# Kernel optimization log

Measured on AMD Instinct MI355X. Metric: run time of the kernel, lower is better.

The kernel has to match this reference:

```python
import jax, jax.numpy as jnp
import numpy as np

N_NODES = 524288
N_EDGES = 2097152
N_GRAPHS = 16384
COMP_DIM = 3539
PROT_DIM = 384
GNN_HID = 64
G_EMB = 128
HID = 256


def setup_inputs() -> dict:
    key = jax.random.key(0)
    ks = jax.random.split(key, 16)
    def lin(k, fan_in, fan_out):
        b = 1.0 / np.sqrt(fan_in)
        kw, kb = jax.random.split(k)
        return (jax.random.uniform(kw, (fan_in, fan_out), jnp.float32, -b, b),
                jax.random.uniform(kb, (fan_out,), jnp.float32, -b, b))
    W1, b1 = lin(ks[0], 1, GNN_HID)
    W2, b2 = lin(ks[1], GNN_HID, GNN_HID)
    Wg, bg = lin(ks[2], GNN_HID, G_EMB)
    Wf1, bf1 = lin(ks[3], G_EMB + COMP_DIM + PROT_DIM, HID)
    Wf2, bf2 = lin(ks[4], HID, 1)
    node_x = jax.random.normal(ks[5], (N_NODES, 1), jnp.float32)
    compound_feat = jax.random.normal(ks[6], (N_GRAPHS, COMP_DIM), jnp.float32)
    protein_feat = jax.random.normal(ks[7], (N_GRAPHS, PROT_DIM), jnp.float32)
    edge_index = jax.random.randint(ks[8], (2, N_EDGES), 0, N_NODES, jnp.int64 if jax.config.jax_enable_x64 else jnp.int32)
    batch = jnp.sort(jax.random.randint(ks[9], (N_NODES,), 0, N_GRAPHS, jnp.int32))
    return {"node_x": node_x, "compound_feat": compound_feat, "protein_feat": protein_feat,
            "edge_index": edge_index, "batch": batch,
            "W1": W1, "b1": b1, "W2": W2, "b2": b2, "Wg": Wg, "bg": bg,
            "Wf1": Wf1, "bf1": bf1, "Wf2": Wf2, "bf2": bf2}


def _gcn_norm(edge_index, num_nodes):
    # add self-loops, then symmetric normalization (PyG GCNConv default)
    loop = jnp.arange(num_nodes, dtype=edge_index.dtype)
    row = jnp.concatenate([edge_index[0], loop])
    col = jnp.concatenate([edge_index[1], loop])
    deg = jax.ops.segment_sum(jnp.ones_like(col, jnp.float32), col, num_segments=num_nodes)
    dinv = jnp.where(deg > 0, jax.lax.rsqrt(deg), 0.0)
    norm = dinv[row] * dinv[col]
    return row, col, norm


def _gcn_conv(x, W, b, row, col, norm, num_nodes):
    h = x @ W  # [N, out]
    out = jax.ops.segment_sum(norm[:, None] * h[row], col, num_segments=num_nodes)
    return out + b


def reference(node_x, compound_feat, protein_feat, edge_index, batch,
              W1, b1, W2, b2, Wg, bg, Wf1, bf1, Wf2, bf2):
    N = node_x.shape[0]
    B = compound_feat.shape[0]
    row, col, norm = _gcn_norm(edge_index, N)
    x = jax.nn.relu(_gcn_conv(node_x, W1, b1, row, col, norm, N))
    x = jax.nn.relu(_gcn_conv(x, W2, b2, row, col, norm, N))
    # global mean pool per graph
    sums = jax.ops.segment_sum(x, batch, num_segments=B)
    cnts = jax.ops.segment_sum(jnp.ones((N,), jnp.float32), batch, num_segments=B)
    pooled = sums / jnp.maximum(cnts, 1.0)[:, None]
    g = pooled @ Wg + bg  # [B, G_EMB]
    combined = jnp.concatenate([g, compound_feat, protein_feat], axis=1)
    h = jax.nn.relu(combined @ Wf1 + bf1)
    return jax.nn.sigmoid(h @ Wf2 + bf2)
```

## Files before the change

kernel.cpp:

```cpp
#include <hip/hip_runtime.h>

#define NN 524288
#define NE 2097152
#define NG 16384
#define CDIM 3539
#define PDIM 384
#define GH 64
#define GE 128
#define HIDD 256
#define KD (GE + CDIM + PDIM)
#define KP 4096

typedef short bf16x8 __attribute__((ext_vector_type(8)));
typedef unsigned short u16x8 __attribute__((ext_vector_type(8)));
typedef float f32x4 __attribute__((ext_vector_type(4)));

__device__ inline unsigned short f2bf(float f) {
    unsigned int u = __float_as_uint(f);
    u += 0x7FFF + ((u >> 16) & 1);
    return (unsigned short)(u >> 16);
}

__global__ void k_init(int* __restrict__ idg, float* __restrict__ sums) {
    int i = blockIdx.x * blockDim.x + threadIdx.x;
    if (i < NN) idg[i] = 0;
    if (i < NG * GH) sums[i] = 0.0f;
}

__global__ void k_deg(const int* __restrict__ ei, int* __restrict__ idg,
                      int* __restrict__ eseq) {
    int e = blockIdx.x * blockDim.x + threadIdx.x;
    eseq[e] = atomicAdd(&idg[ei[NE + e]], 1);
}

__global__ void k_prep(const float* __restrict__ node_x, const int* __restrict__ idg,
                       float2* __restrict__ f2a, int* __restrict__ ecnt) {
    int n = blockIdx.x * blockDim.x + threadIdx.x;
    int c = idg[n];
    float di = rsqrtf((float)(c + 1));
    f2a[n] = make_float2(di * node_x[n], di);
    ecnt[n] = c;
}

__global__ void k_cnt(const int* __restrict__ batch, float* __restrict__ cnt) {
    int g = blockIdx.x * 256 + threadIdx.x;
    int lo = 0, hi = NN;
    while (lo < hi) { int mid = (lo + hi) >> 1; if (batch[mid] < g) lo = mid + 1; else hi = mid; }
    int lo2 = lo, hi2 = NN;
    while (lo2 < hi2) { int mid = (lo2 + hi2) >> 1; if (batch[mid] < g + 1) lo2 = mid + 1; else hi2 = mid; }
    cnt[g] = (float)(lo2 - lo);
}

__global__ void k_scan1(const int* __restrict__ ecnt, int* __restrict__ bsum) {
    __shared__ int ls[256];
    int t = threadIdx.x;
    ls[t] = ecnt[blockIdx.x * 256 + t];
    __syncthreads();
    for (int d = 128; d > 0; d >>= 1) { if (t < d) ls[t] += ls[t + d]; __syncthreads(); }
    if (t == 0) bsum[blockIdx.x] = ls[0];
}

__global__ void k_scan2(int* __restrict__ bsum) {
    __shared__ int ls[256];
    int t = threadIdx.x;
    int loc[8]; int s = 0;
#pragma unroll
    for (int i = 0; i < 8; i++) { loc[i] = bsum[t * 8 + i]; s += loc[i]; }
    ls[t] = s; __syncthreads();
    for (int d = 1; d < 256; d <<= 1) {
        int add = (t >= d) ? ls[t - d] : 0; __syncthreads();
        ls[t] += add; __syncthreads();
    }
    int run = ls[t] - s;
#pragma unroll
    for (int i = 0; i < 8; i++) { int tmp = loc[i]; bsum[t * 8 + i] = run; run += tmp; }
}

__global__ void k_scan3(const int* __restrict__ ecnt, const int* __restrict__ bsum,
                        int* __restrict__ offs) {
    __shared__ int ls[256];
    int t = threadIdx.x, n = blockIdx.x * 256 + t;
    int v = ecnt[n];
    ls[t] = v; __syncthreads();
    for (int d = 1; d < 256; d <<= 1) {
        int add = (t >= d) ? ls[t - d] : 0; __syncthreads();
        ls[t] += add; __syncthreads();
    }
    offs[n] = bsum[blockIdx.x] + ls[t] - v;
    if (n == 0) offs[NN] = NE;
}

__global__ void k_fill(const int* __restrict__ ei, const int* __restrict__ offs,
                       const int* __restrict__ eseq, int* __restrict__ csr) {
    int e = blockIdx.x * 256 + threadIdx.x;
    int r = ei[e], c = ei[NE + e];
    csr[offs[c] + eseq[e]] = r;
}

__global__ void k_sg(const int* __restrict__ offs, const int* __restrict__ csr,
                     const float2* __restrict__ f2a, float2* __restrict__ sd) {
    int n = blockIdx.x * 256 + threadIdx.x;
    int a = offs[n], b = offs[n + 1];
    float2 me = f2a[n];
    float sum = me.x;
    for (int e = a; e < b; e += 8) {
#pragma unroll
        for (int i = 0; i < 8; i++) {
            int ee = e + i;
            int r = csr[min(ee, b - 1)];
            float v = f2a[r].x;
            sum += (ee < b) ? v : 0.0f;
        }
    }
    sd[n] = make_float2(me.y * sum, me.y);
}

__global__ __launch_bounds__(256) void k_gx2(
        const int* __restrict__ offs, const int* __restrict__ csr,
        const float2* __restrict__ sd, const float* __restrict__ W1,
        const float* __restrict__ b1, const unsigned short* __restrict__ W2T,
        const float* __restrict__ b2, const int* __restrict__ batch,
        float* __restrict__ sums) {
    __shared__ __align__(16) char smem[64 * 73 * 4];
    __shared__ int bloc[64];
    unsigned short (*aggs)[72] = (unsigned short (*)[72])smem;
    float (*x2s)[73] = (float (*)[73])smem;
    int t = threadIdx.x;
    int wv = t >> 6, lane = t & 63;
    int n0 = blockIdx.x * 64;
    int nw = n0 + wv * 16;
    if (t < 64) bloc[t] = batch[n0 + t];
    float w1j = W1[lane], b1j = b1[lane];
    int nl = nw + (lane & 15);
    int aL = offs[nl], bndL = offs[nl + 1];
    float2 sdL = sd[nl];

    int base   = __shfl(aL, 0, 64);
    int endAll = __shfl(bndL, 15, 64);

#define LOADB(dst, bs) do { int en = (bs) + lane;                        \
    dst = make_float2(0.0f, 0.0f);                                       \
    if (en < endAll) dst = sd[csr[en]]; } while (0)

    int bstart = base;
    float2 vcur, vnxt;
    LOADB(vcur, bstart);
    LOADB(vnxt, bstart + 64);

    for (int i = 0; i < 16; i++) {
        int a    = __shfl(aL, i, 64);
        int bnd  = __shfl(bndL, i, 64);
        float sx = __shfl(sdL.x, i, 64);
        float sy = __shfl(sdL.y, i, 64);
        float acc = sy * fmaxf(fmaf(sx, w1j, b1j), 0.0f);
        for (int e = a; e < bnd; ++e) {
            int slot = e - bstart;
            if (slot >= 64) {
                bstart += 64;
                slot -= 64;
                vcur = vnxt;
                LOADB(vnxt, bstart + 64);
            }
            float vx = __shfl(vcur.x, slot, 64);
            float vy = __shfl(vcur.y, slot, 64);
            acc = fmaf(vy, fmaxf(fmaf(vx, w1j, b1j), 0.0f), acc);
        }
        aggs[wv * 16 + i][lane] = f2bf(sy * acc);
    }
#undef LOADB

    __syncthreads();
    int lg = lane >> 4, lr = lane & 15;
    bf16x8 a0 = *reinterpret_cast<const bf16x8*>(&aggs[wv * 16 + lr][lg * 8]);
    bf16x8 a1 = *reinterpret_cast<const bf16x8*>(&aggs[wv * 16 + lr][32 + lg * 8]);
    __syncthreads();
    f32x4 acc4[4];
#pragma unroll
    for (int jt = 0; jt < 4; jt++) acc4[jt] = (f32x4){0.f, 0.f, 0.f, 0.f};
#pragma unroll
    for (int jt = 0; jt < 4; jt++) {
        bf16x8 b0 = *reinterpret_cast<const bf16x8*>(W2T + (jt * 16 + lr) * GH + lg * 8);
        bf16x8 b1v = *reinterpret_cast<const bf16x8*>(W2T + (jt * 16 + lr) * GH + 32 + lg * 8);
        acc4[jt] = __builtin_amdgcn_mfma_f32_16x16x32_bf16(a0, b0, acc4[jt], 0, 0, 0);
        acc4[jt] = __builtin_amdgcn_mfma_f32_16x16x32_bf16(a1, b1v, acc4[jt], 0, 0, 0);
    }
#pragma unroll
    for (int jt = 0; jt < 4; jt++) {
        float bj = b2[jt * 16 + lr];
#pragma unroll
        for (int r = 0; r < 4; r++)
            x2s[wv * 16 + lg * 4 + r][jt * 16 + lr] = fmaxf(acc4[jt][r] + bj, 0.0f);
    }
    __syncthreads();
    for (int i = wv; i < 64; i += 4) {
        bool isStart = (i == 0) || (bloc[i] != bloc[i - 1]);
        if (isStart) {
            int g = bloc[i];
            float s = 0.0f;
            int k = i;
            do { s += x2s[k][lane]; k++; } while (k < 64 && bloc[k] == g);
            atomicAdd(&sums[g * GH + lane], s);
        }
    }
}

__global__ void k_graph(const float* __restrict__ sums, const float* __restrict__ cnt,
                        const float* __restrict__ Wg, const float* __restrict__ bg,
                        float* __restrict__ gemb) {
    __shared__ float wgs[GH * GE];
    __shared__ float ps[4 * GH];
    int t = threadIdx.x;
    for (int i = t; i < GH * GE; i += 256) wgs[i] = Wg[i];
    int gid = blockIdx.x * 256 + t;
    int g = gid >> 6, j = t & 63, w = t >> 6;
    float c = fmaxf(cnt[g], 1.0f);
    ps[t] = sums[g * GH + j] / c;
    __syncthreads();
    float o0 = bg[j], o1 = bg[GH + j];
#pragma unroll
    for (int k = 0; k < GH; k++) {
        float p = ps[w * GH + k];
        o0 = fmaf(p, wgs[k * GE + j], o0);
        o1 = fmaf(p, wgs[k * GE + GH + j], o1);
    }
    gemb[g * GE + j] = o0;
    gemb[g * GE + GH + j] = o1;
}

__global__ void k_wt(const float* __restrict__ Wf1, unsigned short* __restrict__ WT,
                     const float* __restrict__ W2, unsigned short* __restrict__ W2T) {
    if (blockIdx.x == 1024) {
        int t = threadIdx.x;
        for (int i = 0; i < 16; i++) {
            int idx = t * 16 + i;
            int j = idx >> 6, k = idx & 63;
            W2T[j * GH + k] = f2bf(W2[k * GH + j]);
        }
        return;
    }
    __shared__ float tl[32][33];
    int bk = blockIdx.x & 127;
    int bn = blockIdx.x >> 7;
    int tx = threadIdx.x & 31, ty = threadIdx.x >> 5;
    int k0 = bk * 32, n0 = bn * 32;
#pragma unroll
    for (int i = 0; i < 4; i++) {
        int k = k0 + ty + i * 8;
        tl[ty + i * 8][tx] = (k < KD) ? Wf1[k * HIDD + n0 + tx] : 0.0f;
    }
    __syncthreads();
#pragma unroll
    for (int i = 0; i < 4; i++) {
        int n = n0 + ty + i * 8;
        WT[n * KP + k0 + tx] = f2bf(tl[tx][ty + i * 8]);
    }
}

__global__ void k_comb(const float* __restrict__ gemb, const float* __restrict__ comp,
                       const float* __restrict__ prot, unsigned short* __restrict__ comb) {
    int idx = blockIdx.x * 256 + threadIdx.x;
    int g = idx >> 9;
    int k0 = (idx & 511) * 8;
    u16x8 r;
    float v[8];
    if (k0 + 8 <= GE) {
        __builtin_memcpy(v, gemb + (size_t)g * GE + k0, 32);
#pragma unroll
        for (int i = 0; i < 8; i++) r[i] = f2bf(v[i]);
    } else if (k0 >= GE && k0 + 8 <= GE + CDIM) {
        __builtin_memcpy(v, comp + (size_t)g * CDIM + (k0 - GE), 32);
#pragma unroll
        for (int i = 0; i < 8; i++) r[i] = f2bf(v[i]);
    } else if (k0 >= GE + CDIM && k0 + 8 <= KD) {
        __builtin_memcpy(v, prot + (size_t)g * PDIM + (k0 - GE - CDIM), 32);
#pragma unroll
        for (int i = 0; i < 8; i++) r[i] = f2bf(v[i]);
    } else if (k0 >= KD) {
#pragma unroll
        for (int i = 0; i < 8; i++) r[i] = 0;
    } else {
#pragma unroll
        for (int i = 0; i < 8; i++) {
            int k = k0 + i;
            float x = 0.0f;
            if (k < GE) x = gemb[g * GE + k];
            else if (k < GE + CDIM) x = comp[(size_t)g * CDIM + (k - GE)];
            else if (k < KD) x = prot[g * PDIM + (k - GE - CDIM)];
            r[i] = f2bf(x);
        }
    }
    *reinterpret_cast<u16x8*>(comb + (size_t)idx * 8) = r;
}

typedef const __attribute__((address_space(1))) void gas_void;
typedef __attribute__((address_space(3))) void las_void;

__global__ __launch_bounds__(256) void k_gemm_mfma(
        const unsigned short* __restrict__ WT, const unsigned short* __restrict__ comb,
        const float* __restrict__ bf1, const float* __restrict__ Wf2,
        const float* __restrict__ bf2, float* __restrict__ out) {
    __shared__ unsigned short ldsA[2][256 * 32];
    __shared__ unsigned short ldsB[2][32 * 32];
    __shared__ float red[32];
    int t = threadIdx.x;
    int wv = t >> 6, lane = t & 63;
    int lg = lane >> 4, lr = lane & 15;
    int g0 = blockIdx.x * 32;
    int nbase = wv * 64;

    int rowp = lane >> 2;
    int kp = (lane & 3) * 8;

    if (t < 32) red[t] = 0.0f;

    f32x4 acc[4][2];
#pragma unroll
    for (int i = 0; i < 4; i++)
#pragma unroll
        for (int j = 0; j < 2; j++) acc[i][j] = (f32x4){0.f, 0.f, 0.f, 0.f};

#define STAGE(buf, k0) do {                                                                  \
    _Pragma("unroll")                                                                        \
    for (int i = 0; i < 4; i++)                                                              \
        __builtin_amdgcn_global_load_lds(                                                    \
            (gas_void*)(WT + (size_t)(wv * 64 + i * 16 + rowp) * KP + (k0) + kp),            \
            (las_void*)(&ldsA[buf][(wv * 64 + i * 16) * 32]), 16, 0, 0);                     \
    if (wv < 2)                                                                              \
        __builtin_amdgcn_global_load_lds(                                                    \
            (gas_void*)(comb + (size_t)(g0 + wv * 16 + rowp) * KP + (k0) + kp),              \
            (las_void*)(&ldsB[buf][(wv * 16) * 32]), 16, 0, 0);                              \
} while (0)

    STAGE(0, 0);
    __syncthreads();
#pragma unroll 1
    for (int s = 0; s < 128; ++s) {
        int cur = s & 1;
        if (s < 127) STAGE(cur ^ 1, (s + 1) * 32);
        bf16x8 a[4], b[2];
#pragma unroll
        for (int nt = 0; nt < 4; nt++)
            a[nt] = *reinterpret_cast<const bf16x8*>(&ldsA[cur][(nbase + nt * 16 + lr) * 32 + lg * 8]);
#pragma unroll
        for (int gt = 0; gt < 2; gt++)
            b[gt] = *reinterpret_cast<const bf16x8*>(&ldsB[cur][(gt * 16 + lr) * 32 + lg * 8]);
#pragma unroll
        for (int nt = 0; nt < 4; nt++)
#pragma unroll
            for (int gt = 0; gt < 2; gt++)
                acc[nt][gt] = __builtin_amdgcn_mfma_f32_16x16x32_bf16(a[nt], b[gt], acc[nt][gt], 0, 0, 0);
        __syncthreads();
    }
#undef STAGE

    float bf2c = bf2[0];
#pragma unroll
    for (int gt = 0; gt < 2; gt++) {
        float pv = 0.0f;
#pragma unroll
        for (int nt = 0; nt < 4; nt++) {
            int nb = nbase + nt * 16 + lg * 4;
#pragma unroll
            for (int r = 0; r < 4; r++) {
                float h = fmaxf(acc[nt][gt][r] + bf1[nb + r], 0.0f);
                pv = fmaf(h, Wf2[nb + r], pv);
            }
        }
        pv += __shfl_xor(pv, 16);
        pv += __shfl_xor(pv, 32);
        if (lane < 16) atomicAdd(&red[gt * 16 + lane], pv);
    }
    __syncthreads();
    if (t < 32) out[g0 + t] = 1.0f / (1.0f + expf(-(red[t] + bf2c)));
}

extern "C" void kernel_launch(void* const* d_in, const int* in_sizes, int n_in,
                              void* d_out, int out_size, void* d_ws, size_t ws_size,
                              hipStream_t stream) {
    const float* node_x = (const float*)d_in[0];
    const float* comp   = (const float*)d_in[1];
    const float* prot   = (const float*)d_in[2];
    const int*   ei     = (const int*)d_in[3];
    const int*   batch  = (const int*)d_in[4];
    const float* W1  = (const float*)d_in[5];
    const float* b1  = (const float*)d_in[6];
    const float* W2  = (const float*)d_in[7];
    const float* b2  = (const float*)d_in[8];
    const float* Wg  = (const float*)d_in[9];
    const float* bg  = (const float*)d_in[10];
    const float* Wf1 = (const float*)d_in[11];
    const float* bf1 = (const float*)d_in[12];
    const float* Wf2 = (const float*)d_in[13];
    const float* bf2 = (const float*)d_in[14];
    float* out = (float*)d_out;

    char* W = (char*)d_ws;
    unsigned short* comb = (unsigned short*)W;
    int*    idg     = (int*)(W + 0);
    float2* f2a     = (float2*)(W + 2097152);
    float2* sd      = (float2*)(W + 6291456);
    int*    ecnt    = (int*)(W + 10485760);
    int*    offs    = (int*)(W + 12582912);
    int*    bsum    = (int*)(W + 16777728);
    int*    csr     = (int*)(W + 16786432);
    float*  sums    = (float*)(W + 25175040);
    float*  cnt     = (float*)(W + 29369344);
    int*    eseq    = (int*)(W + 33554432);
    float*  gemb    = (float*)(W + 134217728);
    unsigned short* WT  = (unsigned short*)(W + 142606336);
    unsigned short* W2T = (unsigned short*)(W + 144703488);

    k_init<<<4096, 256, 0, stream>>>(idg, sums);
    k_wt<<<1025, 256, 0, stream>>>(Wf1, WT, W2, W2T);
    k_deg<<<NE / 256, 256, 0, stream>>>(ei, idg, eseq);
    k_prep<<<NN / 256, 256, 0, stream>>>(node_x, idg, f2a, ecnt);
    k_cnt<<<NG / 256, 256, 0, stream>>>(batch, cnt);
    k_scan1<<<NN / 256, 256, 0, stream>>>(ecnt, bsum);
    k_scan2<<<1, 256, 0, stream>>>(bsum);
    k_scan3<<<NN / 256, 256, 0, stream>>>(ecnt, bsum, offs);
    k_fill<<<NE / 256, 256, 0, stream>>>(ei, offs, eseq, csr);
    k_sg<<<NN / 256, 256, 0, stream>>>(offs, csr, f2a, sd);
    k_gx2<<<NN / 64, 256, 0, stream>>>(offs, csr, sd, W1, b1, W2T, b2, batch, sums);
    k_graph<<<NG * GH / 256, 256, 0, stream>>>(sums, cnt, Wg, bg, gemb);
    k_comb<<<NG * 512 / 256, 256, 0, stream>>>(gemb, comp, prot, comb);
    k_gemm_mfma<<<NG / 32, 256, 0, stream>>>(WT, comb, bf1, Wf2, bf2, out);
}
```

Before: 468.3 us.

## Split final MLP GEMM along K into two halves with separate epilogue kernel

Adds a split-K variant of the fused MLP GEMM that launches twice as many blocks, each reducing half of the 4096-wide K dimension and storing fp32 partial accumulators to workspace. A new finalize kernel sums the two partials and applies bias, ReLU, the second linear layer and sigmoid. The aim is more parallelism and shorter per-block serial loops to better fill the GPU. In exchange it adds a 32 MB partial write and read plus an extra launch, and it only runs if the workspace is large enough.

```diff
diff --git a/kernel.cpp b/kernel.cpp
--- a/kernel.cpp
+++ b/kernel.cpp
@@ -295,31 +295,7 @@
 typedef const __attribute__((address_space(1))) void gas_void;
 typedef __attribute__((address_space(3))) void las_void;
 
-__global__ __launch_bounds__(256) void k_gemm_mfma(
-        const unsigned short* __restrict__ WT, const unsigned short* __restrict__ comb,
-        const float* __restrict__ bf1, const float* __restrict__ Wf2,
-        const float* __restrict__ bf2, float* __restrict__ out) {
-    __shared__ unsigned short ldsA[2][256 * 32];
-    __shared__ unsigned short ldsB[2][32 * 32];
-    __shared__ float red[32];
-    int t = threadIdx.x;
-    int wv = t >> 6, lane = t & 63;
-    int lg = lane >> 4, lr = lane & 15;
-    int g0 = blockIdx.x * 32;
-    int nbase = wv * 64;
-
-    int rowp = lane >> 2;
-    int kp = (lane & 3) * 8;
-
-    if (t < 32) red[t] = 0.0f;
-
-    f32x4 acc[4][2];
-#pragma unroll
-    for (int i = 0; i < 4; i++)
-#pragma unroll
-        for (int j = 0; j < 2; j++) acc[i][j] = (f32x4){0.f, 0.f, 0.f, 0.f};
-
-#define STAGE(buf, k0) do {                                                                  \
+#define GEMM_STAGE(buf, k0) do {                                                             \
     _Pragma("unroll")                                                                        \
     for (int i = 0; i < 4; i++)                                                              \
         __builtin_amdgcn_global_load_lds(                                                    \
@@ -331,12 +307,35 @@
             (las_void*)(&ldsB[buf][(wv * 16) * 32]), 16, 0, 0);                              \
 } while (0)
 
-    STAGE(0, 0);
+__global__ __launch_bounds__(256) void k_gemm_mfma(
+        const unsigned short* __restrict__ WT, const unsigned short* __restrict__ comb,
+        const float* __restrict__ bf1, const float* __restrict__ Wf2,
+        const float* __restrict__ bf2, float* __restrict__ out) {
+    __shared__ unsigned short ldsA[2][256 * 32];
+    __shared__ unsigned short ldsB[2][32 * 32];
+    __shared__ float red[32];
+    int t = threadIdx.x;
+    int wv = t >> 6, lane = t & 63;
+    int lg = lane >> 4, lr = lane & 15;
+    int g0 = blockIdx.x * 32;
+    int nbase = wv * 64;
+    int rowp = lane >> 2;
+    int kp = (lane & 3) * 8;
+
+    if (t < 32) red[t] = 0.0f;
+
+    f32x4 acc[4][2];
+#pragma unroll
+    for (int i = 0; i < 4; i++)
+#pragma unroll
+        for (int j = 0; j < 2; j++) acc[i][j] = (f32x4){0.f, 0.f, 0.f, 0.f};
+
+    GEMM_STAGE(0, 0);
     __syncthreads();
 #pragma unroll 1
     for (int s = 0; s < 128; ++s) {
         int cur = s & 1;
-        if (s < 127) STAGE(cur ^ 1, (s + 1) * 32);
+        if (s < 127) GEMM_STAGE(cur ^ 1, (s + 1) * 32);
         bf16x8 a[4], b[2];
 #pragma unroll
         for (int nt = 0; nt < 4; nt++)
@@ -351,7 +350,6 @@
                 acc[nt][gt] = __builtin_amdgcn_mfma_f32_16x16x32_bf16(a[nt], b[gt], acc[nt][gt], 0, 0, 0);
         __syncthreads();
     }
-#undef STAGE
 
     float bf2c = bf2[0];
 #pragma unroll
@@ -363,6 +361,95 @@
 #pragma unroll
             for (int r = 0; r < 4; r++) {
                 float h = fmaxf(acc[nt][gt][r] + bf1[nb + r], 0.0f);
+                pv = fmaf(h, Wf2[nb + r], pv);
+            }
+        }
+        pv += __shfl_xor(pv, 16);
+        pv += __shfl_xor(pv, 32);
+        if (lane < 16) atomicAdd(&red[gt * 16 + lane], pv);
+    }
+    __syncthreads();
+    if (t < 32) out[g0 + t] = 1.0f / (1.0f + expf(-(red[t] + bf2c)));
+}
+
+__global__ __launch_bounds__(256) void k_gemm_ks(
+        const unsigned short* __restrict__ WT, const unsigned short* __restrict__ comb,
+        float* __restrict__ pacc) {
+    __shared__ unsigned short ldsA[2][256 * 32];
+    __shared__ unsigned short ldsB[2][32 * 32];
+    int t = threadIdx.x;
+    int wv = t >> 6, lane = t & 63;
+    int lg = lane >> 4, lr = lane & 15;
+    int tile = blockIdx.x >> 1, kh = blockIdx.x & 1;
+    int g0 = tile * 32;
+    int kbase = kh * 2048;
+    int nbase = wv * 64;
+    int rowp = lane >> 2;
+    int kp = (lane & 3) * 8;
+
+    f32x4 acc[4][2];
+#pragma unroll
+    for (int i = 0; i < 4; i++)
+#pragma unroll
+        for (int j = 0; j < 2; j++) acc[i][j] = (f32x4){0.f, 0.f, 0.f, 0.f};
+
+    GEMM_STAGE(0, kbase);
+    __syncthreads();
+#pragma unroll 1
+    for (int s = 0; s < 64; ++s) {
+        int cur = s & 1;
+        if (s < 63) GEMM_STAGE(cur ^ 1, kbase + (s + 1) * 32);
+        bf16x8 a[4], b[2];
+#pragma unroll
+        for (int nt = 0; nt < 4; nt++)
+            a[nt] = *reinterpret_cast<const bf16x8*>(&ldsA[cur][(nbase + nt * 16 + lr) * 32 + lg * 8]);
+#pragma unroll
+        for (int gt = 0; gt < 2; gt++)
+            b[gt] = *reinterpret_cast<const bf16x8*>(&ldsB[cur][(gt * 16 + lr) * 32 + lg * 8]);
+#pragma unroll
+        for (int nt = 0; nt < 4; nt++)
+#pragma unroll
+            for (int gt = 0; gt < 2; gt++)
+                acc[nt][gt] = __builtin_amdgcn_mfma_f32_16x16x32_bf16(a[nt], b[gt], acc[nt][gt], 0, 0, 0);
+        __syncthreads();
+    }
+
+    float* dst = pacc + ((size_t)(kh * 512 + tile)) * 8192 + wv * 2048;
+#pragma unroll
+    for (int nt = 0; nt < 4; nt++)
+#pragma unroll
+        for (int gt = 0; gt < 2; gt++)
+            *reinterpret_cast<f32x4*>(dst + (nt * 2 + gt) * 256 + lane * 4) = acc[nt][gt];
+}
+
+__global__ __launch_bounds__(256) void k_fin(
+        const float* __restrict__ pacc, const float* __restrict__ bf1,
+        const float* __restrict__ Wf2, const float* __restrict__ bf2,
+        float* __restrict__ out) {
+    __shared__ float red[32];
+    int t = threadIdx.x;
+    int wv = t >> 6, lane = t & 63;
+    int lg = lane >> 4, lr = lane & 15;
+    int tile = blockIdx.x;
+    int g0 = tile * 32;
+    int nbase = wv * 64;
+    if (t < 32) red[t] = 0.0f;
+    __syncthreads();
+    float bf2c = bf2[0];
+    const float* p0 = pacc + (size_t)tile * 8192 + wv * 2048;
+    const float* p1 = pacc + (size_t)(512 + tile) * 8192 + wv * 2048;
+#pragma unroll
+    for (int gt = 0; gt < 2; gt++) {
+        float pv = 0.0f;
+#pragma unroll
+        for (int nt = 0; nt < 4; nt++) {
+            int idx = (nt * 2 + gt) * 256 + lane * 4;
+            f32x4 a0 = *reinterpret_cast<const f32x4*>(p0 + idx);
+            f32x4 a1 = *reinterpret_cast<const f32x4*>(p1 + idx);
+            int nb = nbase + nt * 16 + lg * 4;
+#pragma unroll
+            for (int r = 0; r < 4; r++) {
+                float h = fmaxf(a0[r] + a1[r] + bf1[nb + r], 0.0f);
                 pv = fmaf(h, Wf2[nb + r], pv);
             }
         }
@@ -409,6 +496,8 @@
     float*  gemb    = (float*)(W + 134217728);
     unsigned short* WT  = (unsigned short*)(W + 142606336);
     unsigned short* W2T = (unsigned short*)(W + 144703488);
+    float*  pacc    = (float*)(W + 144711680);
+    bool ks = (ws_size >= 144711680ULL + 33554432ULL);
 
     k_init<<<4096, 256, 0, stream>>>(idg, sums);
     k_wt<<<1025, 256, 0, stream>>>(Wf1, WT, W2, W2T);
@@ -423,5 +512,10 @@
     k_gx2<<<NN / 64, 256, 0, stream>>>(offs, csr, sd, W1, b1, W2T, b2, batch, sums);
     k_graph<<<NG * GH / 256, 256, 0, stream>>>(sums, cnt, Wg, bg, gemb);
     k_comb<<<NG * 512 / 256, 256, 0, stream>>>(gemb, comp, prot, comb);
-    k_gemm_mfma<<<NG / 32, 256, 0, stream>>>(WT, comb, bf1, Wf2, bf2, out);
-}
+    if (ks) {
+        k_gemm_ks<<<1024, 256, 0, stream>>>(WT, comb, pacc);
+        k_fin<<<512, 256, 0, stream>>>(pacc, bf1, Wf2, bf2, out);
+    } else {
+        k_gemm_mfma<<<NG / 32, 256, 0, stream>>>(WT, comb, bf1, Wf2, bf2, out);
+    }
+}
```

Measured after the change: 476.7 us. Within noise of the previous version (+1.8%).
